# Kernel optimization log

Hardware: AMD Instinct MI355X
Metric: run time of the kernel (lower is better)

The kernel has to match this reference:

```python
import jax, jax.numpy as jnp
import numpy as np

IN_F = 512
OUT_F = 512

def setup_inputs() -> dict:
    key = jax.random.key(0)
    k1, k2, k3 = jax.random.split(key, 3)
    x = jax.random.normal(k1, (2, 512, IN_F), dtype=jnp.float32)
    # uniform init: a = sqrt(6 / (2 + out_features))
    a = float(np.sqrt(6.0 / (2.0 + OUT_F)))
    W = jax.random.uniform(k2, (OUT_F, IN_F), dtype=jnp.float32, minval=-a, maxval=a)
    bound = float(1.0 / np.sqrt(IN_F))
    b = jax.random.uniform(k3, (OUT_F,), dtype=jnp.float32, minval=-bound, maxval=bound)
    return {"x": x, "W": W, "b": b}

def reference(x, W, b):
    # MAM fully connected (beta == 0 path): for each (row, out-neuron),
    # C = max_k(x_k * w_ok) + min_k(x_k * w_ok), then add bias.
    xf = x.reshape(-1, x.shape[-1])            # (B, in)
    prod = xf[:, None, :] * W[None, :, :]      # (B, out, in) -- the large intermediate
    C = prod.max(axis=-1) + prod.min(axis=-1)  # (B, out)
    C = C + b[None, :]
    return C.reshape(x.shape[:-1] + (W.shape[0],))
```

## Files before the change

### kernel.cpp

```cpp
#include <hip/hip_runtime.h>
#include <math.h>


#define O_TOTAL 512
#define K_TOTAL 512
#define OBLK 64
#define NWAVE 4
#define RPW 4
#define RPB (NWAVE * RPW)
#define KCH 64
#define NCHUNK (K_TOTAL / KCH)
#define NJ (KCH / 4)

__device__ __forceinline__ void stage16(const float* g, float* lds_base) {
#if __has_builtin(__builtin_amdgcn_global_load_lds)
  __builtin_amdgcn_global_load_lds(
      (__attribute__((address_space(1))) unsigned int*)g,
      (__attribute__((address_space(3))) unsigned int*)lds_base, 16, 0, 0);
#else
  *reinterpret_cast<float4*>(lds_base + (threadIdx.x & 63) * 4) =
      *reinterpret_cast<const float4*>(g);
#endif
}

__global__ __launch_bounds__(256, 2)
void mam_fc_kernel(const float* __restrict__ x, const float* __restrict__ W,
                   const float* __restrict__ bias, float* __restrict__ out) {
  __shared__ __align__(16) float Wl[2][OBLK * KCH];

  const int t = threadIdx.x;
  const int lane = t & 63;
  const int wv = __builtin_amdgcn_readfirstlane(t >> 6);
  const int ob = blockIdx.x & 7;
  const int rg = blockIdx.x >> 3;
  const int o0 = ob * OBLK;
  const int rowBase = rg * RPB + wv * RPW;

  const float* srcW[4];
  int dstWoff[4];
#pragma unroll
  for (int p = 0; p < 4; ++p) {
    const int orow = wv * 16 + p * 4 + (lane >> 4);
    const int g = (lane & 15) ^ (orow & 15);
    srcW[p] = W + (size_t)(o0 + orow) * K_TOTAL + g * 4;
    dstWoff[p] = (wv * 16 + p * 4) * KCH;
  }

  const float* xr = x + (size_t)rowBase * K_TOTAL;

  float amax[RPW], amin[RPW];
#pragma unroll
  for (int r = 0; r < RPW; ++r) { amax[r] = -INFINITY; amin[r] = INFINITY; }

  const unsigned baseW = (unsigned)(lane * (KCH * 4) + (lane & 15) * 16);

#pragma unroll
  for (int p = 0; p < 4; ++p) stage16(srcW[p], &Wl[0][dstWoff[p]]);

#pragma unroll 1
  for (int c = 0; c < NCHUNK; ++c) {
    __syncthreads();

    if (c + 1 < NCHUNK) {
      const int kOff = (c + 1) * KCH;
#pragma unroll
      for (int p = 0; p < 4; ++p)
        stage16(srcW[p] + kOff, &Wl[(c + 1) & 1][dstWoff[p]]);
    }

    const char* wb = (const char*)&Wl[c & 1][0];
    float4 w[NJ];
#pragma unroll
    for (int j = 0; j < NJ; ++j)
      w[j] = *reinterpret_cast<const float4*>(wb + (baseW ^ (unsigned)(j * 16)));

#pragma unroll
    for (int r = 0; r < RPW; ++r) {
      const float* xrc = xr + (size_t)r * K_TOTAL + c * KCH;
#pragma unroll
      for (int j = 0; j < NJ; ++j) {
        const float4 xv = *reinterpret_cast<const float4*>(xrc + j * 4);
        const float p0 = xv.x * w[j].x;
        const float p1 = xv.y * w[j].y;
        const float p2 = xv.z * w[j].z;
        const float p3 = xv.w * w[j].w;
        amax[r] = fmaxf(fmaxf(fmaxf(fmaxf(amax[r], p0), p1), p2), p3);
        amin[r] = fminf(fminf(fminf(fminf(amin[r], p0), p1), p2), p3);
      }
    }
  }

  const float bv = bias[o0 + lane];
#pragma unroll
  for (int r = 0; r < RPW; ++r) {
    out[(size_t)(rowBase + r) * O_TOTAL + o0 + lane] =
        amax[r] + amin[r] + bv;
  }
}

extern "C" void kernel_launch(void* const* d_in, const int* in_sizes, int n_in,
                              void* d_out, int out_size, void* d_ws, size_t ws_size,
                              hipStream_t stream) {
  const float* x = (const float*)d_in[0];
  const float* W = (const float*)d_in[1];
  const float* b = (const float*)d_in[2];
  float* out = (float*)d_out;

  const int nrows = in_sizes[0] / K_TOTAL;
  const int nblocks = (O_TOTAL / OBLK) * (nrows / RPB);
  mam_fc_kernel<<<dim3(nblocks), dim3(256), 0, stream>>>(x, W, b, out);
}
```

Before: 25.17 us.

## Split K across wave pairs with LDS reduction and double the block count

Each block now handles 8 rows instead of 16. Within a block, two waves share the same rows and each takes one half of K, and their max/min partials are merged through shared memory at the end. This doubles the grid from 512 to 1024 blocks to raise occupancy on the many CUs, and halves the per-wave serial loop. The weight chunk shrinks to 32 columns but covers both K halves, with a new 8-way swizzle. The cost is an extra LDS reduction and barrier, and the weight tile is reused across fewer rows per block, so each weight is loaded more times overall.

```diff
diff --git a/kernel.cpp b/kernel.cpp
--- a/kernel.cpp
+++ b/kernel.cpp
@@ -5,11 +5,10 @@
 #define O_TOTAL 512
 #define K_TOTAL 512
 #define OBLK 64
-#define NWAVE 4
+#define KHALF 256
+#define KCH 32
+#define NPH (KHALF / KCH)
 #define RPW 4
-#define RPB (NWAVE * RPW)
-#define KCH 64
-#define NCHUNK (K_TOTAL / KCH)
 #define NJ (KCH / 4)
 
 __device__ __forceinline__ void stage16(const float* g, float* lds_base) {
@@ -23,10 +22,11 @@
 #endif
 }
 
-__global__ __launch_bounds__(256, 2)
+__global__ __launch_bounds__(256, 4)
 void mam_fc_kernel(const float* __restrict__ x, const float* __restrict__ W,
                    const float* __restrict__ bias, float* __restrict__ out) {
-  __shared__ __align__(16) float Wl[2][OBLK * KCH];
+  __shared__ __align__(16) float Wl[2][2 * OBLK * KCH];
+  __shared__ float red[2][RPW][64][2];
 
   const int t = threadIdx.x;
   const int lane = t & 63;
@@ -34,67 +34,78 @@
   const int ob = blockIdx.x & 7;
   const int rg = blockIdx.x >> 3;
   const int o0 = ob * OBLK;
-  const int rowBase = rg * RPB + wv * RPW;
+  const int pair = wv >> 1;
+  const int half = wv & 1;
+  const int rowBase = rg * 8 + pair * RPW;
+  const int kBase = half * KHALF;
 
   const float* srcW[4];
-  int dstWoff[4];
+  int dstOff[4];
 #pragma unroll
-  for (int p = 0; p < 4; ++p) {
-    const int orow = wv * 16 + p * 4 + (lane >> 4);
-    const int g = (lane & 15) ^ (orow & 15);
-    srcW[p] = W + (size_t)(o0 + orow) * K_TOTAL + g * 4;
-    dstWoff[p] = (wv * 16 + p * 4) * KCH;
+  for (int i = 0; i < 4; ++i) {
+    const int s = wv * 4 + i;
+    const int h = s >> 3;
+    const int so = s & 7;
+    const int orow = so * 8 + (lane >> 3);
+    const int g = (lane & 7) ^ (orow & 7);
+    srcW[i] = W + (size_t)(o0 + orow) * K_TOTAL + h * KHALF + g * 4;
+    dstOff[i] = h * (OBLK * KCH) + so * 256;
   }
-
-  const float* xr = x + (size_t)rowBase * K_TOTAL;
 
   float amax[RPW], amin[RPW];
 #pragma unroll
   for (int r = 0; r < RPW; ++r) { amax[r] = -INFINITY; amin[r] = INFINITY; }
 
-  const unsigned baseW = (unsigned)(lane * (KCH * 4) + (lane & 15) * 16);
+  const unsigned baseW = (unsigned)(lane * (KCH * 4) + (lane & 7) * 16);
+  const float* xw = x + (size_t)rowBase * K_TOTAL + kBase;
 
 #pragma unroll
-  for (int p = 0; p < 4; ++p) stage16(srcW[p], &Wl[0][dstWoff[p]]);
+  for (int i = 0; i < 4; ++i) stage16(srcW[i], &Wl[0][dstOff[i]]);
 
 #pragma unroll 1
-  for (int c = 0; c < NCHUNK; ++c) {
+  for (int p = 0; p < NPH; ++p) {
     __syncthreads();
 
-    if (c + 1 < NCHUNK) {
-      const int kOff = (c + 1) * KCH;
+    if (p + 1 < NPH) {
 #pragma unroll
-      for (int p = 0; p < 4; ++p)
-        stage16(srcW[p] + kOff, &Wl[(c + 1) & 1][dstWoff[p]]);
+      for (int i = 0; i < 4; ++i)
+        stage16(srcW[i] + (p + 1) * KCH, &Wl[(p + 1) & 1][dstOff[i]]);
     }
 
-    const char* wb = (const char*)&Wl[c & 1][0];
-    float4 w[NJ];
+    const char* wb = (const char*)&Wl[p & 1][half * (OBLK * KCH)];
+    const float* xp = xw + p * KCH;
 #pragma unroll
-    for (int j = 0; j < NJ; ++j)
-      w[j] = *reinterpret_cast<const float4*>(wb + (baseW ^ (unsigned)(j * 16)));
-
+    for (int j = 0; j < NJ; ++j) {
+      const float4 w4 = *reinterpret_cast<const float4*>(wb + (baseW ^ (unsigned)(j * 16)));
 #pragma unroll
-    for (int r = 0; r < RPW; ++r) {
-      const float* xrc = xr + (size_t)r * K_TOTAL + c * KCH;
-#pragma unroll
-      for (int j = 0; j < NJ; ++j) {
-        const float4 xv = *reinterpret_cast<const float4*>(xrc + j * 4);
-        const float p0 = xv.x * w[j].x;
-        const float p1 = xv.y * w[j].y;
-        const float p2 = xv.z * w[j].z;
-        const float p3 = xv.w * w[j].w;
+      for (int r = 0; r < RPW; ++r) {
+        const float4 xv = *reinterpret_cast<const float4*>(xp + (size_t)r * K_TOTAL + j * 4);
+        const float p0 = xv.x * w4.x;
+        const float p1 = xv.y * w4.y;
+        const float p2 = xv.z * w4.z;
+        const float p3 = xv.w * w4.w;
         amax[r] = fmaxf(fmaxf(fmaxf(fmaxf(amax[r], p0), p1), p2), p3);
         amin[r] = fminf(fminf(fminf(fminf(amin[r], p0), p1), p2), p3);
       }
     }
   }
 
-  const float bv = bias[o0 + lane];
+  if (half) {
 #pragma unroll
-  for (int r = 0; r < RPW; ++r) {
-    out[(size_t)(rowBase + r) * O_TOTAL + o0 + lane] =
-        amax[r] + amin[r] + bv;
+    for (int r = 0; r < RPW; ++r) {
+      red[pair][r][lane][0] = amax[r];
+      red[pair][r][lane][1] = amin[r];
+    }
+  }
+  __syncthreads();
+  if (!half) {
+    const float bv = bias[o0 + lane];
+#pragma unroll
+    for (int r = 0; r < RPW; ++r) {
+      const float m = fmaxf(amax[r], red[pair][r][lane][0]);
+      const float n = fminf(amin[r], red[pair][r][lane][1]);
+      out[(size_t)(rowBase + r) * O_TOTAL + o0 + lane] = m + n + bv;
+    }
   }
 }
 
@@ -107,6 +118,6 @@
   float* out = (float*)d_out;
 
   const int nrows = in_sizes[0] / K_TOTAL;
-  const int nblocks = (O_TOTAL / OBLK) * (nrows / RPB);
+  const int nblocks = (O_TOTAL / OBLK) * (nrows / 8);
   mam_fc_kernel<<<dim3(nblocks), dim3(256), 0, stream>>>(x, W, b, out);
 }
```

Measured after the change: 21.24 us. 15.6% less time.
